# Kernel tuning notes

Measured on AMD Instinct MI355X. Metric: run time of the kernel, lower is better.

The kernel has to match this reference:

```python
import jax, jax.numpy as jnp
import numpy as np

N, E, IN_DIM, OUT_DIM, H = 50000, 800000, 128, 16, 8


def setup_inputs() -> dict:
    key = jax.random.key(0)
    ks = jax.random.split(key, 10)
    h = jax.random.normal(ks[0], (N, IN_DIM), dtype=jnp.float32)
    row = jnp.sort(jax.random.randint(ks[1], (E,), 0, N))
    col = jax.random.randint(ks[2], (E,), 0, N)
    s = 1.0 / np.sqrt(IN_DIM)
    Wq = jax.random.normal(ks[3], (IN_DIM, OUT_DIM * H), dtype=jnp.float32) * s
    Wk = jax.random.normal(ks[4], (IN_DIM, OUT_DIM * H), dtype=jnp.float32) * s
    Wv = jax.random.normal(ks[5], (IN_DIM, OUT_DIM * H), dtype=jnp.float32) * s
    bq = jnp.zeros((OUT_DIM * H,), jnp.float32)
    bk = jnp.zeros((OUT_DIM * H,), jnp.float32)
    bv = jnp.zeros((OUT_DIM * H,), jnp.float32)
    return {"h": h, "Wq": Wq, "bq": bq, "Wk": Wk, "bk": bk, "Wv": Wv, "bv": bv,
            "row": row, "col": col}


def reference(h, Wq, bq, Wk, bk, Wv, bv, row, col):
    n = h.shape[0]
    scaling = OUT_DIM ** (-0.5)
    # projections, reshaped (N, out_dim, heads) as in the torch module
    q = (h @ Wq + bq).reshape(n, OUT_DIM, H) * scaling
    k = (h @ Wk + bk).reshape(n, OUT_DIM, H)
    v = (h @ Wv + bv).reshape(n, OUT_DIM, H)
    # bsddmm: per-edge, per-head dot product  score[e,h] = <q[row[e],:,h], k[col[e],:,h]>
    s = jnp.einsum('edh,edh->eh', q[row], k[col])  # [E, H]
    # sparse row-wise softmax (over each destination node's neighbors)
    m = jax.ops.segment_max(s, row, num_segments=n)       # [N, H]
    p = jnp.exp(s - m[row])                               # [E, H]
    z = jax.ops.segment_sum(p, row, num_segments=n)       # [N, H]
    attn = p / z[row]                                     # [E, H]
    # bspmm: out[i,d,h] = sum_{e: row[e]=i} attn[e,h] * v[col[e],d,h]
    out = jax.ops.segment_sum(attn[:, None, :] * v[col], row, num_segments=n)
    return out.reshape(n, -1)
```

## Files before the change

kernel.cpp:

```cpp
#include <hip/hip_runtime.h>
#include <math.h>

typedef unsigned int uint32;
typedef _Float16 f16x8 __attribute__((ext_vector_type(8)));
typedef _Float16 f16x2 __attribute__((ext_vector_type(2)));
typedef float f32x4 __attribute__((ext_vector_type(4)));

union frag_u { f16x8 h; uint32 u[4]; uint4 q; };


__device__ __forceinline__ uint32 pack_f16(float lo, float hi) {
    auto r = __builtin_amdgcn_cvt_pkrtz(lo, hi);
    return __builtin_bit_cast(uint32, r);
}
__device__ __forceinline__ float dot2acc(uint32 a, uint32 b, float c) {
#if __has_builtin(__builtin_amdgcn_fdot2)
    return __builtin_amdgcn_fdot2(__builtin_bit_cast(f16x2, a),
                                  __builtin_bit_cast(f16x2, b), c, false);
#else
    f16x2 av = __builtin_bit_cast(f16x2, a), bv = __builtin_bit_cast(f16x2, b);
    return fmaf((float)av[0], (float)bv[0], fmaf((float)av[1], (float)bv[1], c));
#endif
}

__global__ __launch_bounds__(256) void prep_kernel(
    const float* __restrict__ Wq, const float* __restrict__ Wk,
    const float* __restrict__ Wv, uint32* __restrict__ Wt,
    const int* __restrict__ row, int* __restrict__ rp, int N, int E)
{
    const int t = threadIdx.x;
    if (blockIdx.x < 3) {
        __shared__ unsigned short tile[128][129];
        const int m = blockIdx.x;
        const float* W = (m == 0) ? Wq : (m == 1) ? Wk : Wv;
        const float4* W4 = reinterpret_cast<const float4*>(W);
        #pragma unroll
        for (int i0 = 0; i0 < 16; ++i0) {
            int i = t + i0 * 256;
            int k = i >> 5, nq = i & 31;
            float4 v = W4[i];
            tile[nq * 4 + 0][k] = (unsigned short)(pack_f16(v.x, 0.f) & 0xFFFFu);
            tile[nq * 4 + 1][k] = (unsigned short)(pack_f16(v.y, 0.f) & 0xFFFFu);
            tile[nq * 4 + 2][k] = (unsigned short)(pack_f16(v.z, 0.f) & 0xFFFFu);
            tile[nq * 4 + 3][k] = (unsigned short)(pack_f16(v.w, 0.f) & 0xFFFFu);
        }
        __syncthreads();
        uint32* out = Wt + (size_t)m * 8192;
        #pragma unroll
        for (int i0 = 0; i0 < 32; ++i0) {
            int i = t + i0 * 256;
            int n = i >> 6, kp = i & 63;
            out[i] = (uint32)tile[n][kp * 2] | ((uint32)tile[n][kp * 2 + 1] << 16);
        }
    } else {
        int i = (blockIdx.x - 3) * 256 + t;
        if (i > N) return;
        int lo = 0, hi = E;
        while (lo < hi) {
            int mid = (lo + hi) >> 1;
            if (row[mid] < i) lo = mid + 1; else hi = mid;
        }
        rp[i] = lo;
    }
}

__global__ __launch_bounds__(256) void proj_mfma_kernel(
    const float* __restrict__ h, const uint32* __restrict__ Wt,
    const float* __restrict__ bq, const float* __restrict__ bk,
    const float* __restrict__ bv,
    uint32* __restrict__ Qp, uint2* __restrict__ KV, int N)
{
    const int t = threadIdx.x;
    const int lane = t & 63;
    const int w = t >> 6;
    const int r = lane & 15, g = lane >> 4;
    const int nbase = blockIdx.x * 64;

    frag_u afr[4][4];
    const float4* h4 = reinterpret_cast<const float4*>(h);
    #pragma unroll
    for (int ng = 0; ng < 4; ++ng) {
        int arow = nbase + ng * 16 + r;
        bool av = arow < N;
        #pragma unroll
        for (int kb = 0; kb < 4; ++kb) {
            float4 x = make_float4(0.f,0.f,0.f,0.f), y = x;
            if (av) {
                size_t base = (size_t)arow * 32 + (kb * 4 + g) * 2;
                x = h4[base]; y = h4[base + 1];
            }
            afr[ng][kb].u[0] = pack_f16(x.x, x.y);
            afr[ng][kb].u[1] = pack_f16(x.z, x.w);
            afr[ng][kb].u[2] = pack_f16(y.x, y.y);
            afr[ng][kb].u[3] = pack_f16(y.z, y.w);
        }
    }

    const float SCALE_Q = 0.25f * 1.44269504f;
    const int c = w * 16 + r;
    uint32 kpk[4][4];

    #pragma unroll
    for (int mat = 0; mat < 3; ++mat) {
        const uint32* wb = Wt + mat * 8192;
        frag_u bfr[2][4];
        #pragma unroll
        for (int tti = 0; tti < 2; ++tti)
            #pragma unroll
            for (int kb = 0; kb < 4; ++kb)
                bfr[tti][kb].q = *reinterpret_cast<const uint4*>(
                    wb + ((w + 4 * tti) * 16 + r) * 64 + (kb * 4 + g) * 4);

        f32x4 acc[4][2];
        #pragma unroll
        for (int ng = 0; ng < 4; ++ng)
            #pragma unroll
            for (int tti = 0; tti < 2; ++tti)
                acc[ng][tti] = (f32x4){0.f, 0.f, 0.f, 0.f};

        #pragma unroll
        for (int ng = 0; ng < 4; ++ng)
            #pragma unroll
            for (int tti = 0; tti < 2; ++tti)
                #pragma unroll
                for (int kb = 0; kb < 4; ++kb)
                    acc[ng][tti] = __builtin_amdgcn_mfma_f32_16x16x32_f16(
                        afr[ng][kb].h, bfr[tti][kb].h, acc[ng][tti], 0, 0, 0);

        const float* bias = (mat == 0) ? bq : (mat == 1) ? bk : bv;
        float blo = bias[c], bhi = bias[c + 64];
        #pragma unroll
        for (int ng = 0; ng < 4; ++ng) {
            #pragma unroll
            for (int reg = 0; reg < 4; ++reg) {
                int node = nbase + ng * 16 + g * 4 + reg;
                float lo = acc[ng][0][reg] + blo;
                float hi = acc[ng][1][reg] + bhi;
                if (mat == 0) {
                    if (node < N)
                        Qp[(size_t)node * 64 + c] = pack_f16(lo * SCALE_Q, hi * SCALE_Q);
                } else if (mat == 1) {
                    kpk[ng][reg] = pack_f16(lo, hi);
                } else {
                    if (node < N)
                        KV[(size_t)node * 64 + c] = make_uint2(kpk[ng][reg], pack_f16(lo, hi));
                }
            }
        }
    }
}

__global__ __launch_bounds__(256) void edge_attn_kernel(
    const uint32* __restrict__ Qp, const uint2* __restrict__ KV,
    const int* __restrict__ rp, const int* __restrict__ col,
    float* __restrict__ out, int N)
{
    const int lane = threadIdx.x & 63;
    const int node = blockIdx.x * 4 + (threadIdx.x >> 6);
    if (node >= N) return;
    const int hh   = lane & 7;
    const int slot = lane >> 3;

    const int start = rp[node], end = rp[node + 1];
    float* outp = out + (size_t)node * 128;
    if (start >= end) { outp[lane] = 0.f; outp[lane + 64] = 0.f; return; }
    const int last = end - 1;

    uint32 q[8];
    {
        const uint32* qrow = Qp + (size_t)node * 64;
        #pragma unroll
        for (int i = 0; i < 8; ++i) q[i] = qrow[hh + 8 * i];
    }

    float z = 0.f;
    float acc[16];
    #pragma unroll
    for (int i = 0; i < 16; ++i) acc[i] = 0.f;

    uint2 bufA[8], bufB[8];
    #define LOADG(buf, c0) { \
        const uint2* kvr = KV + (size_t)(c0) * 64; \
        _Pragma("unroll") \
        for (int i = 0; i < 8; ++i) (buf)[i] = kvr[hh + 8 * i]; }
    #define PROC(buf, gb) { \
        float s = 0.f; \
        _Pragma("unroll") \
        for (int i = 0; i < 8; ++i) s = dot2acc(q[i], (buf)[i].x, s); \
        float p = ((gb) + slot < end) ? __builtin_amdgcn_exp2f(s) : 0.f; \
        z += p; \
        _Pragma("unroll") \
        for (int i = 0; i < 8; ++i) { \
            f16x2 hv = __builtin_bit_cast(f16x2, (buf)[i].y); \
            acc[i]     = fmaf(p, (float)hv[0], acc[i]); \
            acc[8 + i] = fmaf(p, (float)hv[1], acc[8 + i]); } }

    int cA = col[min(start + slot, last)];
    int cB = col[min(start + 8 + slot, last)];
    LOADG(bufA, cA);
    int gb = start;
    while (true) {
        LOADG(bufB, cB);
        cA = col[min(gb + 16 + slot, last)];
        PROC(bufA, gb);
        gb += 8;
        if (gb >= end) break;
        LOADG(bufA, cA);
        cB = col[min(gb + 16 + slot, last)];
        PROC(bufB, gb);
        gb += 8;
        if (gb >= end) break;
    }

    #pragma unroll
    for (int m = 8; m <= 32; m <<= 1) {
        z += __shfl_xor(z, m);
        #pragma unroll
        for (int i = 0; i < 16; ++i) acc[i] += __shfl_xor(acc[i], m);
    }

    const float rz = 1.0f / z;
    outp[lane]      = acc[slot] * rz;
    outp[lane + 64] = acc[8 + slot] * rz;
}

extern "C" void kernel_launch(void* const* d_in, const int* in_sizes, int n_in,
                              void* d_out, int out_size, void* d_ws, size_t ws_size,
                              hipStream_t stream)
{
    const float* h  = (const float*)d_in[0];
    const float* Wq = (const float*)d_in[1];
    const float* bq = (const float*)d_in[2];
    const float* Wk = (const float*)d_in[3];
    const float* bk = (const float*)d_in[4];
    const float* Wv = (const float*)d_in[5];
    const float* bv = (const float*)d_in[6];
    const int* row  = (const int*)d_in[7];
    const int* col  = (const int*)d_in[8];
    float* out = (float*)d_out;

    const int N = in_sizes[0] / 128;
    const int E = in_sizes[7];

    uint2*  KV = (uint2*)d_ws;
    uint32* Qp = (uint32*)(KV + (size_t)N * 64);
    uint32* Wt = Qp + (size_t)N * 64;
    int*    rp = (int*)(Wt + 3 * 8192);

    const int rp_blocks = (N + 1 + 255) / 256;
    prep_kernel<<<3 + rp_blocks, 256, 0, stream>>>(Wq, Wk, Wv, Wt, row, rp, N, E);
    proj_mfma_kernel<<<(N + 63) / 64, 256, 0, stream>>>(
        h, Wt, bq, bk, bv, Qp, KV, N);
    edge_attn_kernel<<<(N + 3) / 4, 256, 0, stream>>>(Qp, KV, rp, col, out, N);
}
```

Baseline: 103.8 us.

## Move row-pointer search into projection kernel and retile projection per wave

The binary search building row pointers moves out of the weight-transpose kernel into extra blocks of the projection kernel, so the small prep kernel launches only three blocks. The projection now gives each wave its own 32 rows across all output column tiles instead of sharing 64 rows across four waves. Each wave therefore reloads all B fragments, but fewer A fragments are held in registers, which may help occupancy. The edge-attention kernel also drops to 128-thread blocks of two nodes each, for finer scheduling granularity.

```diff
diff --git a/kernel.cpp b/kernel.cpp
--- a/kernel.cpp
+++ b/kernel.cpp
@@ -25,35 +25,44 @@
 
 __global__ __launch_bounds__(256) void prep_kernel(
     const float* __restrict__ Wq, const float* __restrict__ Wk,
-    const float* __restrict__ Wv, uint32* __restrict__ Wt,
-    const int* __restrict__ row, int* __restrict__ rp, int N, int E)
+    const float* __restrict__ Wv, uint32* __restrict__ Wt)
 {
     const int t = threadIdx.x;
-    if (blockIdx.x < 3) {
-        __shared__ unsigned short tile[128][129];
-        const int m = blockIdx.x;
-        const float* W = (m == 0) ? Wq : (m == 1) ? Wk : Wv;
-        const float4* W4 = reinterpret_cast<const float4*>(W);
-        #pragma unroll
-        for (int i0 = 0; i0 < 16; ++i0) {
-            int i = t + i0 * 256;
-            int k = i >> 5, nq = i & 31;
-            float4 v = W4[i];
-            tile[nq * 4 + 0][k] = (unsigned short)(pack_f16(v.x, 0.f) & 0xFFFFu);
-            tile[nq * 4 + 1][k] = (unsigned short)(pack_f16(v.y, 0.f) & 0xFFFFu);
-            tile[nq * 4 + 2][k] = (unsigned short)(pack_f16(v.z, 0.f) & 0xFFFFu);
-            tile[nq * 4 + 3][k] = (unsigned short)(pack_f16(v.w, 0.f) & 0xFFFFu);
-        }
-        __syncthreads();
-        uint32* out = Wt + (size_t)m * 8192;
-        #pragma unroll
-        for (int i0 = 0; i0 < 32; ++i0) {
-            int i = t + i0 * 256;
-            int n = i >> 6, kp = i & 63;
-            out[i] = (uint32)tile[n][kp * 2] | ((uint32)tile[n][kp * 2 + 1] << 16);
-        }
-    } else {
-        int i = (blockIdx.x - 3) * 256 + t;
+    __shared__ unsigned short tile[128][129];
+    const int m = blockIdx.x;
+    const float* W = (m == 0) ? Wq : (m == 1) ? Wk : Wv;
+    const float4* W4 = reinterpret_cast<const float4*>(W);
+    #pragma unroll
+    for (int i0 = 0; i0 < 16; ++i0) {
+        int i = t + i0 * 256;
+        int k = i >> 5, nq = i & 31;
+        float4 v = W4[i];
+        tile[nq * 4 + 0][k] = (unsigned short)(pack_f16(v.x, 0.f) & 0xFFFFu);
+        tile[nq * 4 + 1][k] = (unsigned short)(pack_f16(v.y, 0.f) & 0xFFFFu);
+        tile[nq * 4 + 2][k] = (unsigned short)(pack_f16(v.z, 0.f) & 0xFFFFu);
+        tile[nq * 4 + 3][k] = (unsigned short)(pack_f16(v.w, 0.f) & 0xFFFFu);
+    }
+    __syncthreads();
+    uint32* out = Wt + (size_t)m * 8192;
+    #pragma unroll
+    for (int i0 = 0; i0 < 32; ++i0) {
+        int i = t + i0 * 256;
+        int n = i >> 6, kp = i & 63;
+        out[i] = (uint32)tile[n][kp * 2] | ((uint32)tile[n][kp * 2 + 1] << 16);
+    }
+}
+
+__global__ __launch_bounds__(256) void proj_mfma_kernel(
+    const float* __restrict__ h, const uint32* __restrict__ Wt,
+    const float* __restrict__ bq, const float* __restrict__ bk,
+    const float* __restrict__ bv,
+    uint32* __restrict__ Qp, uint2* __restrict__ KV,
+    const int* __restrict__ row, int* __restrict__ rp,
+    int N, int E, int PB)
+{
+    const int t = threadIdx.x;
+    if ((int)blockIdx.x >= PB) {
+        int i = ((int)blockIdx.x - PB) * 256 + t;
         if (i > N) return;
         int lo = 0, hi = E;
         while (lo < hi) {
@@ -61,26 +70,19 @@
             if (row[mid] < i) lo = mid + 1; else hi = mid;
         }
         rp[i] = lo;
-    }
-}
-
-__global__ __launch_bounds__(256) void proj_mfma_kernel(
-    const float* __restrict__ h, const uint32* __restrict__ Wt,
-    const float* __restrict__ bq, const float* __restrict__ bk,
-    const float* __restrict__ bv,
-    uint32* __restrict__ Qp, uint2* __restrict__ KV, int N)
-{
-    const int t = threadIdx.x;
+        return;
+    }
+
     const int lane = t & 63;
     const int w = t >> 6;
     const int r = lane & 15, g = lane >> 4;
-    const int nbase = blockIdx.x * 64;
-
-    frag_u afr[4][4];
+    const int rbase = blockIdx.x * 128 + w * 32;
+
+    frag_u afr[2][4];
     const float4* h4 = reinterpret_cast<const float4*>(h);
     #pragma unroll
-    for (int ng = 0; ng < 4; ++ng) {
-        int arow = nbase + ng * 16 + r;
+    for (int ng = 0; ng < 2; ++ng) {
+        int arow = rbase + ng * 16 + r;
         bool av = arow < N;
         #pragma unroll
         for (int kb = 0; kb < 4; ++kb) {
@@ -97,66 +99,69 @@
     }
 
     const float SCALE_Q = 0.25f * 1.44269504f;
-    const int c = w * 16 + r;
-    uint32 kpk[4][4];
-
-    #pragma unroll
-    for (int mat = 0; mat < 3; ++mat) {
-        const uint32* wb = Wt + mat * 8192;
-        frag_u bfr[2][4];
-        #pragma unroll
-        for (int tti = 0; tti < 2; ++tti)
-            #pragma unroll
-            for (int kb = 0; kb < 4; ++kb)
-                bfr[tti][kb].q = *reinterpret_cast<const uint4*>(
-                    wb + ((w + 4 * tti) * 16 + r) * 64 + (kb * 4 + g) * 4);
-
-        f32x4 acc[4][2];
-        #pragma unroll
-        for (int ng = 0; ng < 4; ++ng)
+
+    #pragma unroll
+    for (int tp = 0; tp < 4; ++tp) {
+        const int c = tp * 16 + r;
+        uint32 kpk[2][4];
+        #pragma unroll
+        for (int mat = 0; mat < 3; ++mat) {
+            const uint32* wb = Wt + mat * 8192;
+            frag_u bfr[2][4];
             #pragma unroll
             for (int tti = 0; tti < 2; ++tti)
-                acc[ng][tti] = (f32x4){0.f, 0.f, 0.f, 0.f};
-
-        #pragma unroll
-        for (int ng = 0; ng < 4; ++ng)
-            #pragma unroll
-            for (int tti = 0; tti < 2; ++tti)
                 #pragma unroll
                 for (int kb = 0; kb < 4; ++kb)
-                    acc[ng][tti] = __builtin_amdgcn_mfma_f32_16x16x32_f16(
-                        afr[ng][kb].h, bfr[tti][kb].h, acc[ng][tti], 0, 0, 0);
-
-        const float* bias = (mat == 0) ? bq : (mat == 1) ? bk : bv;
-        float blo = bias[c], bhi = bias[c + 64];
-        #pragma unroll
-        for (int ng = 0; ng < 4; ++ng) {
-            #pragma unroll
-            for (int reg = 0; reg < 4; ++reg) {
-                int node = nbase + ng * 16 + g * 4 + reg;
-                float lo = acc[ng][0][reg] + blo;
-                float hi = acc[ng][1][reg] + bhi;
-                if (mat == 0) {
-                    if (node < N)
-                        Qp[(size_t)node * 64 + c] = pack_f16(lo * SCALE_Q, hi * SCALE_Q);
-                } else if (mat == 1) {
-                    kpk[ng][reg] = pack_f16(lo, hi);
-                } else {
-                    if (node < N)
-                        KV[(size_t)node * 64 + c] = make_uint2(kpk[ng][reg], pack_f16(lo, hi));
+                    bfr[tti][kb].q = *reinterpret_cast<const uint4*>(
+                        wb + ((tp + 4 * tti) * 16 + r) * 64 + (kb * 4 + g) * 4);
+
+            f32x4 acc[2][2];
+            #pragma unroll
+            for (int ng = 0; ng < 2; ++ng)
+                #pragma unroll
+                for (int tti = 0; tti < 2; ++tti)
+                    acc[ng][tti] = (f32x4){0.f, 0.f, 0.f, 0.f};
+
+            #pragma unroll
+            for (int ng = 0; ng < 2; ++ng)
+                #pragma unroll
+                for (int tti = 0; tti < 2; ++tti)
+                    #pragma unroll
+                    for (int kb = 0; kb < 4; ++kb)
+                        acc[ng][tti] = __builtin_amdgcn_mfma_f32_16x16x32_f16(
+                            afr[ng][kb].h, bfr[tti][kb].h, acc[ng][tti], 0, 0, 0);
+
+            const float* bias = (mat == 0) ? bq : (mat == 1) ? bk : bv;
+            float blo = bias[c], bhi = bias[c + 64];
+            #pragma unroll
+            for (int ng = 0; ng < 2; ++ng) {
+                #pragma unroll
+                for (int reg = 0; reg < 4; ++reg) {
+                    int node = rbase + ng * 16 + g * 4 + reg;
+                    float lo = acc[ng][0][reg] + blo;
+                    float hi = acc[ng][1][reg] + bhi;
+                    if (mat == 0) {
+                        if (node < N)
+                            Qp[(size_t)node * 64 + c] = pack_f16(lo * SCALE_Q, hi * SCALE_Q);
+                    } else if (mat == 1) {
+                        kpk[ng][reg] = pack_f16(lo, hi);
+                    } else {
+                        if (node < N)
+                            KV[(size_t)node * 64 + c] = make_uint2(kpk[ng][reg], pack_f16(lo, hi));
+                    }
                 }
             }
         }
     }
 }
 
-__global__ __launch_bounds__(256) void edge_attn_kernel(
+__global__ __launch_bounds__(128) void edge_attn_kernel(
     const uint32* __restrict__ Qp, const uint2* __restrict__ KV,
     const int* __restrict__ rp, const int* __restrict__ col,
     float* __restrict__ out, int N)
 {
     const int lane = threadIdx.x & 63;
-    const int node = blockIdx.x * 4 + (threadIdx.x >> 6);
+    const int node = blockIdx.x * 2 + (threadIdx.x >> 6);
     if (node >= N) return;
     const int hh   = lane & 7;
     const int slot = lane >> 3;
@@ -247,9 +252,11 @@
     uint32* Wt = Qp + (size_t)N * 64;
     int*    rp = (int*)(Wt + 3 * 8192);
 
+    const int PB = (N + 127) / 128;
     const int rp_blocks = (N + 1 + 255) / 256;
-    prep_kernel<<<3 + rp_blocks, 256, 0, stream>>>(Wq, Wk, Wv, Wt, row, rp, N, E);
-    proj_mfma_kernel<<<(N + 63) / 64, 256, 0, stream>>>(
-        h, Wt, bq, bk, bv, Qp, KV, N);
-    edge_attn_kernel<<<(N + 3) / 4, 256, 0, stream>>>(Qp, KV, rp, col, out, N);
-}
+
+    prep_kernel<<<3, 256, 0, stream>>>(Wq, Wk, Wv, Wt);
+    proj_mfma_kernel<<<PB + rp_blocks, 256, 0, stream>>>(
+        h, Wt, bq, bk, bv, Qp, KV, row, rp, N, E, PB);
+    edge_attn_kernel<<<(N + 1) / 2, 128, 0, stream>>>(Qp, KV, rp, col, out, N);
+}
```

Measured after the change: 102.1 us. Within noise of the previous version (-1.6%).
